# Performance work log

Measured on AMD Instinct MI355X. Metric: run time of the kernel, lower is better.

The kernel has to match this reference:

```python
import jax, jax.numpy as jnp
import numpy as np

T, B, V, E, H = 512, 64, 50000, 256, 256  # seq, batch, vocab, embed, lstm_hidden
D2 = 2 * H
NC = 5


def setup_inputs() -> dict:
    key = jax.random.key(0)
    ks = jax.random.split(key, 16)
    u = lambda k, shape, s=0.1: jax.random.uniform(k, shape, jnp.float32, -s, s)
    return {
        "embed": jax.random.randint(ks[0], (T, B), 0, V),
        "h0": jnp.zeros((2, B, H), jnp.float32),
        "c0": jnp.zeros((2, B, H), jnp.float32),
        "emb_table": jax.random.normal(ks[1], (V, E), jnp.float32),
        "Wih_f": u(ks[2], (4 * H, E)),
        "Whh_f": u(ks[3], (4 * H, H)),
        "bih_f": u(ks[4], (4 * H,)),
        "bhh_f": u(ks[5], (4 * H,)),
        "Wih_b": u(ks[6], (4 * H, E)),
        "Whh_b": u(ks[7], (4 * H, H)),
        "bih_b": u(ks[8], (4 * H,)),
        "bhh_b": u(ks[9], (4 * H,)),
        "W_word": u(ks[10], (D2, D2)),
        "b_word": u(ks[11], (D2,)),
        "proj_word": u(ks[12], (D2,)),
        "lin_W": u(ks[13], (NC, D2)),
        "lin_b": u(ks[14], (NC,)),
    }


def _lstm_dir(x, h0, c0, Wih, Whh, bih, bhh):
    # x: (T,B,E). PyTorch LSTM gate order: i, f, g, o.
    xg = jnp.einsum('tbe,ge->tbg', x, Wih) + bih + bhh  # (T,B,4H)

    def step(carry, xt):
        h, c = carry
        g = xt + h @ Whh.T
        i, f, gg, o = jnp.split(g, 4, axis=-1)
        c = jax.nn.sigmoid(f) * c + jax.nn.sigmoid(i) * jnp.tanh(gg)
        h = jax.nn.sigmoid(o) * jnp.tanh(c)
        return (h, c), h

    _, hs = jax.lax.scan(step, (h0, c0), xg)
    return hs  # (T,B,H)


def reference(embed, h0, c0, emb_table,
              Wih_f, Whh_f, bih_f, bhh_f,
              Wih_b, Whh_b, bih_b, bhh_b,
              W_word, b_word, proj_word, lin_W, lin_b):
    x = emb_table[embed]  # (T,B,E)
    out_f = _lstm_dir(x, h0[0], c0[0], Wih_f, Whh_f, bih_f, bhh_f)
    out_b = _lstm_dir(x[::-1], h0[1], c0[1], Wih_b, Whh_b, bih_b, bhh_b)[::-1]
    out = jnp.concatenate([out_f, out_b], axis=-1)  # (T,B,2H)
    # additive attention: tanh(out @ W + b) @ proj, softmax over T
    squish = jnp.tanh(jnp.einsum('tbd,de->tbe', out, W_word) + b_word)
    attn = jax.nn.softmax(jnp.einsum('tbd,d->tb', squish, proj_word), axis=0)
    vec = jnp.einsum('tb,tbd->bd', attn, out)  # (B,2H)
    return vec @ lin_W.T + lin_b  # (B, n_classes)
```

## Files before the change

kernel.cpp:

```cpp
#include <hip/hip_runtime.h>
#include <hip/hip_fp16.h>
#include <cstdint>
#include <cstddef>

#define TT 512
#define BB 64
#define EE 256
#define HH 256
#define G4 1024
#define DD 512
#define NCLS 5
#define CH 64
#define NCH (TT / CH)

typedef _Float16 half8 __attribute__((ext_vector_type(8)));
typedef float f32x4 __attribute__((ext_vector_type(4)));

#define OFF_XGF   0ull
#define OFF_XGB   8388608ull
#define OFF_OUTB  16777216ull
#define OFF_WHHF  50331648ull
#define OFF_WIHF  51380224ull
#define OFF_BIAS  52428800ull
#define OFF_HST   52436992ull
#define OFF_CST   52568064ull
#define OFF_LOG   52699136ull
#define OFF_ATT   52830208ull
#define OFF_HEX   52961280ull
#define OFF_FLG   53092352ull

__device__ __forceinline__ f32x4 mfma16(half8 a, half8 b, f32x4 c) {
  return __builtin_amdgcn_mfma_f32_16x16x32_f16(a, b, c, 0, 0, 0);
}
__device__ __forceinline__ f32x4 shflx4(f32x4 v, int mask) {
  f32x4 r;
  r[0] = __shfl_xor(v[0], mask, 64);
  r[1] = __shfl_xor(v[1], mask, 64);
  r[2] = __shfl_xor(v[2], mask, 64);
  r[3] = __shfl_xor(v[3], mask, 64);
  return r;
}

#define HSWZ(br, u) ((((br) * 256) + (u)) ^ (((br) & 7) << 3))

__global__ __launch_bounds__(256) void make_frags(
    const float* __restrict__ WhhF, const float* __restrict__ WhhB,
    const float* __restrict__ WihF, const float* __restrict__ WihB,
    __half* __restrict__ whhfrag, __half* __restrict__ wihfrag)
{
  int idx = blockIdx.x * 256 + threadIdx.x;
  int r = idx & 7, lane = (idx >> 3) & 63, ks = (idx >> 9) & 7;
  int mm = lane & 15;
  int k = ks * 32 + (lane >> 4) * 8 + r;
  if (idx < (1 << 19)) {
    int pf = (idx >> 12) & 63, d = (idx >> 18) & 1;
    const float* W = d ? WhhB : WhhF;
    int g = (mm & 3) * 256 + pf * 4 + (mm >> 2);
    whhfrag[idx] = __float2half(W[(size_t)g * HH + k]);
  } else {
    int e = idx - (1 << 19);
    int pf = (e >> 12) & 63, d = (e >> 18) & 1;
    const float* W = d ? WihB : WihF;
    int g = (mm & 3) * 256 + pf * 4 + (mm >> 2);
    wihfrag[e] = __float2half(W[(size_t)g * EE + k]);
  }
}

__global__ __launch_bounds__(256) void bias_prep(
    const float* __restrict__ bihF, const float* __restrict__ bhhF,
    const float* __restrict__ bihB, const float* __restrict__ bhhB,
    float* __restrict__ bias)
{
  int i = blockIdx.x * 256 + threadIdx.x;
  int d = i >> 10, pcol = i & 1023;
  int g = (pcol & 3) * 256 + (pcol >> 2);
  bias[i] = (d ? bihB : bihF)[g] + (d ? bhhB : bhhF)[g];
}

__global__ __launch_bounds__(256) void xg_mfma(
    int c, const int* __restrict__ embed, const float* __restrict__ emb,
    const __half* __restrict__ wihfrag, const float* __restrict__ biassum,
    __half* __restrict__ xgF, __half* __restrict__ xgB)
{
  const int d = blockIdx.z, ls = blockIdx.x, gblk = blockIdx.y;
  int t = c * CH + ls;
  if (d) t = TT - 1 - t;
  __half* xg = d ? xgB : xgF;
  const int tid = threadIdx.x, w = tid >> 6, l = tid & 63;

  __shared__ int idx[64];
  __shared__ unsigned short xs[64 * 256];

  if (tid < 64) idx[tid] = embed[t * BB + tid];
  __syncthreads();

  {
    const int rr = tid >> 2, cq = (tid & 3) * 64;
    const float* src = emb + (size_t)idx[rr] * EE + cq;
#pragma unroll
    for (int j = 0; j < 8; ++j) {
      float4 a = *(const float4*)(src + j * 8);
      float4 b = *(const float4*)(src + j * 8 + 4);
      half8 hv;
      hv[0] = (_Float16)a.x; hv[1] = (_Float16)a.y; hv[2] = (_Float16)a.z; hv[3] = (_Float16)a.w;
      hv[4] = (_Float16)b.x; hv[5] = (_Float16)b.y; hv[6] = (_Float16)b.z; hv[7] = (_Float16)b.w;
      int hidx = (rr * 256 + cq + j * 8) ^ ((rr & 7) << 3);
      *(half8*)&xs[hidx] = hv;
    }
  }
  __syncthreads();

  const __half* bfb = wihfrag + (size_t)((d * 64 + gblk * 4) * 8) * 512 + l * 8;
  half8 Bf[4][8];
#pragma unroll
  for (int ct = 0; ct < 4; ++ct)
#pragma unroll
    for (int ks = 0; ks < 8; ++ks)
      Bf[ct][ks] = *(const half8*)(bfb + (ct * 8 + ks) * 512);

  f32x4 acc[4];
#pragma unroll
  for (int ct = 0; ct < 4; ++ct) {
    float bv = biassum[d * 1024 + gblk * 64 + ct * 16 + (l & 15)];
    acc[ct][0] = bv; acc[ct][1] = bv; acc[ct][2] = bv; acc[ct][3] = bv;
  }

  const int arow = w * 16 + (l & 15);
#pragma unroll
  for (int ks = 0; ks < 8; ++ks) {
    int hidx = (arow * 256 + ks * 32 + (l >> 4) * 8) ^ ((arow & 7) << 3);
    half8 af = *(const half8*)&xs[hidx];
#pragma unroll
    for (int ct = 0; ct < 4; ++ct)
      acc[ct] = mfma16(af, Bf[ct][ks], acc[ct]);
  }

#pragma unroll
  for (int ct = 0; ct < 4; ++ct) {
    ushort4 sv;
    sv.x = __half_as_ushort(__float2half(acc[ct][0]));
    sv.y = __half_as_ushort(__float2half(acc[ct][1]));
    sv.z = __half_as_ushort(__float2half(acc[ct][2]));
    sv.w = __half_as_ushort(__float2half(acc[ct][3]));
    size_t base = ((size_t)(ls * 4 + w) * 64 + (gblk * 4 + ct)) * 256 + l * 4;
    *(ushort4*)((unsigned short*)xg + base) = sv;
  }
}

__global__ __launch_bounds__(512, 2) void scan_dist4(
    int c, const __half* __restrict__ xgF, const __half* __restrict__ xgB,
    const __half* __restrict__ whhfrag,
    const float* __restrict__ hin, const float* __restrict__ cin,
    float* __restrict__ hstate, float* __restrict__ cstate,
    __half* __restrict__ outb, unsigned long long* __restrict__ hexu,
    int* __restrict__ flags)
{
  const int id = blockIdx.x;
  const int ug = id >> 3, grp = id & 7;
  const int d = grp >> 2, bg = grp & 3;
  const int tid = threadIdx.x, w = tid >> 6, l = tid & 63;
  const int m = l & 15, qr = l >> 4, q = m & 3, ul = m >> 2;
  const unsigned short* xg = (const unsigned short*)(d ? xgB : xgF);

  __shared__ unsigned short hb0[16 * 256];
  __shared__ unsigned short hb1[16 * 256];

  const int pf0 = ug * 16 + w * 2;

  half8 Wf[2][8];
#pragma unroll
  for (int cf = 0; cf < 2; ++cf)
#pragma unroll
    for (int ks = 0; ks < 8; ++ks)
      Wf[cf][ks] = *(const half8*)(whhfrag +
          ((size_t)(d * 64 + pf0 + cf) * 8 + ks) * 512 + l * 8);

#pragma unroll
  for (int i = 0; i < 8; ++i) {
    int idx = i * 512 + tid;
    int r = idx >> 8, u = idx & 255;
    hb0[HSWZ(r, u)] = __half_as_ushort(
        __float2half(hin[(size_t)(d * BB + bg * 16 + r) * HH + u]));
  }
  float cst[2][4];
#pragma unroll
  for (int cf = 0; cf < 2; ++cf) {
    int U = (pf0 + cf) * 4 + ul;
#pragma unroll
    for (int j = 0; j < 4; ++j)
      cst[cf][j] = cin[(size_t)(d * BB + bg * 16 + qr * 4 + j) * HH + U];
  }
  __syncthreads();

  int afo[8];
#pragma unroll
  for (int ks = 0; ks < 8; ++ks) afo[ks] = HSWZ(m, ks * 32 + qr * 8);
  const int kso0 = ug * 2, kso1 = ug * 2 + 1;

  const unsigned short* xp = xg + ((size_t)bg * 64 + pf0) * 256 + l * 4;
  const float actB = (q == 2) ? 2.f : 1.f;

  f32x4 acc[2];
  {
    ushort4 xv0[2];
#pragma unroll
    for (int cf = 0; cf < 2; ++cf) xv0[cf] = *(const ushort4*)(xp + cf * 256);
#pragma unroll
    for (int cf = 0; cf < 2; ++cf) {
      acc[cf][0] = __half2float(__ushort_as_half(xv0[cf].x));
      acc[cf][1] = __half2float(__ushort_as_half(xv0[cf].y));
      acc[cf][2] = __half2float(__ushort_as_half(xv0[cf].z));
      acc[cf][3] = __half2float(__ushort_as_half(xv0[cf].w));
    }
    half8 ao0 = *(const half8*)&hb0[afo[kso0]];
    half8 ao1 = *(const half8*)&hb0[afo[kso1]];
#pragma unroll
    for (int cf = 0; cf < 2; ++cf) {
      acc[cf] = mfma16(ao0, Wf[cf][kso0], acc[cf]);
      acc[cf] = mfma16(ao1, Wf[cf][kso1], acc[cf]);
    }
  }
  ushort4 xv[2];
#pragma unroll
  for (int cf = 0; cf < 2; ++cf)
    xv[cf] = *(const ushort4*)(xp + (size_t)65536 + cf * 256);

  int p = 0;
  for (int ls = 0; ls < CH; ++ls) {
    unsigned short* cur = p ? hb1 : hb0;
    unsigned short* nxt = p ? hb0 : hb1;
    int tA = c * CH + ls;
    if (d) tA = TT - 1 - tA;
    unsigned long long* hx = hexu + (size_t)(grp * 2 + (ls & 1)) * 1024;

    half8 afp[6];
#pragma unroll
    for (int i = 0; i < 6; ++i) {
      int ks = i + (i >= kso0 ? 2 : 0);
      afp[i] = *(const half8*)&cur[afo[ks]];
    }
#pragma unroll
    for (int i = 0; i < 6; ++i) {
      int ks = i + (i >= kso0 ? 2 : 0);
#pragma unroll
      for (int cf = 0; cf < 2; ++cf)
        acc[cf] = mfma16(afp[i], Wf[cf][ks], acc[cf]);
    }

#pragma unroll
    for (int cf = 0; cf < 2; ++cf) {
      f32x4 a0;
#pragma unroll
      for (int jj = 0; jj < 4; ++jj) {
        float e = __expf(actB * acc[cf][jj]);
        a0[jj] = 1.f - __fdividef(actB, e + 1.f);
      }
      f32x4 a1 = shflx4(a0, 1);
      f32x4 a2 = shflx4(a0, 2);
      f32x4 a3 = shflx4(a0, 3);
      const int U = (pf0 + cf) * 4 + ul;
      float hv[4];
#pragma unroll
      for (int jj = 0; jj < 4; ++jj) {
        float cn = a1[jj] * cst[cf][jj] + a0[jj] * a2[jj];
        cst[cf][jj] = cn;
        float e2 = __expf(2.f * cn);
        hv[jj] = a3[jj] * (1.f - __fdividef(2.f, e2 + 1.f));
      }
      if (q == 0) {
        unsigned int p0 = (unsigned int)__half_as_ushort(__float2half(hv[0])) |
            ((unsigned int)__half_as_ushort(__float2half(hv[1])) << 16);
        unsigned int p1 = (unsigned int)__half_as_ushort(__float2half(hv[2])) |
            ((unsigned int)__half_as_ushort(__float2half(hv[3])) << 16);
        nxt[HSWZ(qr * 4 + 0, U)] = (unsigned short)(p0 & 0xffff);
        nxt[HSWZ(qr * 4 + 1, U)] = (unsigned short)(p0 >> 16);
        nxt[HSWZ(qr * 4 + 2, U)] = (unsigned short)(p1 & 0xffff);
        nxt[HSWZ(qr * 4 + 3, U)] = (unsigned short)(p1 >> 16);
        unsigned long long pk =
            (unsigned long long)p0 | ((unsigned long long)p1 << 32);
        __hip_atomic_store(&hx[U * 4 + qr], pk, __ATOMIC_RELAXED,
                           __HIP_MEMORY_SCOPE_AGENT);
      }
    }
    asm volatile("s_waitcnt vmcnt(0)" ::: "memory");
    __syncthreads();

    const int fbase = ((grp * NCH + c) * CH + ls) * 32;
    if (tid == 0)
      __hip_atomic_store(&flags[fbase + ug], 1, __ATOMIC_RELAXED,
                         __HIP_MEMORY_SCOPE_AGENT);

    {
      const int pr = tid >> 5, uL2 = (tid & 31) * 2;
      const int u = ug * 64 + uL2;
      *(unsigned int*)&outb[((size_t)tA * BB + bg * 16 + pr) * DD + d * HH + u] =
          *(const unsigned int*)&nxt[HSWZ(pr, u)];
    }
#pragma unroll
    for (int cf = 0; cf < 2; ++cf) {
      acc[cf][0] = __half2float(__ushort_as_half(xv[cf].x));
      acc[cf][1] = __half2float(__ushort_as_half(xv[cf].y));
      acc[cf][2] = __half2float(__ushort_as_half(xv[cf].z));
      acc[cf][3] = __half2float(__ushort_as_half(xv[cf].w));
    }
    {
      half8 ao0 = *(const half8*)&nxt[afo[kso0]];
      half8 ao1 = *(const half8*)&nxt[afo[kso1]];
#pragma unroll
      for (int cf = 0; cf < 2; ++cf) {
        acc[cf] = mfma16(ao0, Wf[cf][kso0], acc[cf]);
        acc[cf] = mfma16(ao1, Wf[cf][kso1], acc[cf]);
      }
    }
    {
      int lsn = (ls + 2 < CH) ? ls + 2 : CH - 1;
      const unsigned short* xn = xp + (size_t)lsn * 65536;
#pragma unroll
      for (int cf = 0; cf < 2; ++cf)
        xv[cf] = *(const ushort4*)(xn + cf * 256);
    }

    {
      bool need = (l < 4) && (l != ug);
      int got = need ? 0 : 1;
      while (!__all(got != 0)) {
        if (need && !got)
          got = __hip_atomic_load(&flags[fbase + l], __ATOMIC_RELAXED,
                                  __HIP_MEMORY_SCOPE_AGENT);
      }
    }
#pragma unroll
    for (int rep = 0; rep < 2; ++rep) {
      int idx = tid + rep * 512;
      if (idx < 768) {
        int pi = idx >> 8, rem = idx & 255, uu = rem >> 2, rq = rem & 3;
        int peer = pi + (pi >= ug ? 1 : 0);
        int U = peer * 64 + uu;
        unsigned long long v =
            __hip_atomic_load(&hx[U * 4 + rq], __ATOMIC_RELAXED,
                              __HIP_MEMORY_SCOPE_AGENT);
        nxt[HSWZ(rq * 4 + 0, U)] = (unsigned short)(v & 0xffff);
        nxt[HSWZ(rq * 4 + 1, U)] = (unsigned short)((v >> 16) & 0xffff);
        nxt[HSWZ(rq * 4 + 2, U)] = (unsigned short)((v >> 32) & 0xffff);
        nxt[HSWZ(rq * 4 + 3, U)] = (unsigned short)(v >> 48);
      }
    }
    __syncthreads();
    p ^= 1;
  }

  {
    unsigned short* fin = p ? hb1 : hb0;
#pragma unroll
    for (int i = 0; i < 8; ++i) {
      int idx = i * 512 + tid;
      int r = idx >> 8, u = idx & 255;
      hstate[(size_t)(d * BB + bg * 16 + r) * HH + u] =
          __half2float(__ushort_as_half(fin[HSWZ(r, u)]));
    }
  }
  if (q == 0) {
#pragma unroll
    for (int cf = 0; cf < 2; ++cf) {
      int U = (pf0 + cf) * 4 + ul;
#pragma unroll
      for (int j = 0; j < 4; ++j)
        cstate[(size_t)(d * BB + bg * 16 + qr * 4 + j) * HH + U] = cst[cf][j];
    }
  }
}

__global__ __launch_bounds__(1024, 1) void squish_logits(
    const __half* __restrict__ outb, const float* __restrict__ Ww,
    const float* __restrict__ bw, const float* __restrict__ proj,
    float* __restrict__ logits)
{
  const int r0 = blockIdx.x * 64;
  const int tid = threadIdx.x;
  const int tm = tid >> 6;
  const int tn = tid & 63;
  __shared__ float As[16][68];
  __shared__ float Bs[16][516];
  __shared__ float red[64][65];

  float acc[4][8] = {};
  const int am = tid >> 4, ak = tid & 15;
  const int bk = tid >> 7, bn = (tid & 127) * 4;

  for (int k0 = 0; k0 < DD; k0 += 16) {
    float a0 = __half2float(outb[(size_t)(r0 + am) * DD + k0 + ak]);
    float4 b0 = *(const float4*)&Ww[(size_t)(k0 + bk) * DD + bn];
    float4 b1 = *(const float4*)&Ww[(size_t)(k0 + bk + 8) * DD + bn];
    __syncthreads();
    As[ak][am] = a0;
    *(float4*)&Bs[bk][bn] = b0;
    *(float4*)&Bs[bk + 8][bn] = b1;
    __syncthreads();
#pragma unroll
    for (int k = 0; k < 16; ++k) {
      float4 a = *(const float4*)&As[k][tm * 4];
      float4 p0 = *(const float4*)&Bs[k][tn * 8];
      float4 p1 = *(const float4*)&Bs[k][tn * 8 + 4];
      float av[4] = {a.x, a.y, a.z, a.w};
#pragma unroll
      for (int i = 0; i < 4; ++i) {
        acc[i][0] += av[i] * p0.x; acc[i][1] += av[i] * p0.y;
        acc[i][2] += av[i] * p0.z; acc[i][3] += av[i] * p0.w;
        acc[i][4] += av[i] * p1.x; acc[i][5] += av[i] * p1.y;
        acc[i][6] += av[i] * p1.z; acc[i][7] += av[i] * p1.w;
      }
    }
  }
  float partial[4] = {0.f, 0.f, 0.f, 0.f};
#pragma unroll
  for (int jj = 0; jj < 8; ++jj) {
    int col = tn * 8 + jj;
    float bwv = bw[col], pv = proj[col];
#pragma unroll
    for (int i = 0; i < 4; ++i)
      partial[i] += tanhf(acc[i][jj] + bwv) * pv;
  }
#pragma unroll
  for (int i = 0; i < 4; ++i) red[tm * 4 + i][tn] = partial[i];
  __syncthreads();
  if (tid < 64) {
    float s = 0.f;
    for (int x = 0; x < 64; ++x) s += red[tid][x];
    logits[r0 + tid] = s;
  }
}

__global__ __launch_bounds__(256) void softmax_t(const float* __restrict__ logits,
                                                 float* __restrict__ attn)
{
  const int b = blockIdx.x;
  const int tid = threadIdx.x;
  __shared__ float sm[256];
  float v0 = logits[tid * BB + b];
  float v1 = logits[(tid + 256) * BB + b];
  sm[tid] = fmaxf(v0, v1);
  __syncthreads();
  for (int s = 128; s > 0; s >>= 1) {
    if (tid < s) sm[tid] = fmaxf(sm[tid], sm[tid + s]);
    __syncthreads();
  }
  float M = sm[0];
  __syncthreads();
  float e0 = expf(v0 - M), e1 = expf(v1 - M);
  sm[tid] = e0 + e1;
  __syncthreads();
  for (int s = 128; s > 0; s >>= 1) {
    if (tid < s) sm[tid] += sm[tid + s];
    __syncthreads();
  }
  float inv = 1.f / sm[0];
  attn[tid * BB + b] = e0 * inv;
  attn[(tid + 256) * BB + b] = e1 * inv;
}

__global__ __launch_bounds__(512) void vec_final(
    const __half* __restrict__ outb, const float* __restrict__ attn,
    const float* __restrict__ linW, const float* __restrict__ linb,
    float* __restrict__ y)
{
  const int b = blockIdx.x;
  const int d = threadIdx.x;
  float acc = 0.f;
  for (int t = 0; t < TT; ++t)
    acc += attn[t * BB + b] * __half2float(outb[((size_t)t * BB + b) * DD + d]);
  __shared__ float red[512];
  for (int cls = 0; cls < NCLS; ++cls) {
    red[d] = acc * linW[cls * DD + d];
    __syncthreads();
    for (int s = 256; s > 0; s >>= 1) {
      if (d < s) red[d] += red[d + s];
      __syncthreads();
    }
    if (d == 0) y[b * NCLS + cls] = red[0] + linb[cls];
    __syncthreads();
  }
}

extern "C" void kernel_launch(void* const* d_in, const int* in_sizes, int n_in,
                              void* d_out, int out_size, void* d_ws, size_t ws_size,
                              hipStream_t stream) {
  const int*   embed     = (const int*)d_in[0];
  const float* h0        = (const float*)d_in[1];
  const float* c0        = (const float*)d_in[2];
  const float* emb_table = (const float*)d_in[3];
  const float* Wih_f     = (const float*)d_in[4];
  const float* Whh_f     = (const float*)d_in[5];
  const float* bih_f     = (const float*)d_in[6];
  const float* bhh_f     = (const float*)d_in[7];
  const float* Wih_b     = (const float*)d_in[8];
  const float* Whh_b     = (const float*)d_in[9];
  const float* bih_b     = (const float*)d_in[10];
  const float* bhh_b     = (const float*)d_in[11];
  const float* W_word    = (const float*)d_in[12];
  const float* b_word    = (const float*)d_in[13];
  const float* proj_word = (const float*)d_in[14];
  const float* lin_W     = (const float*)d_in[15];
  const float* lin_b     = (const float*)d_in[16];

  char* ws = (char*)d_ws;
  __half* xgF     = (__half*)(ws + OFF_XGF);
  __half* xgB     = (__half*)(ws + OFF_XGB);
  __half* outb    = (__half*)(ws + OFF_OUTB);
  __half* whhfrag = (__half*)(ws + OFF_WHHF);
  __half* wihfrag = (__half*)(ws + OFF_WIHF);
  float*  biassum = (float*)(ws + OFF_BIAS);
  float*  hstate  = (float*)(ws + OFF_HST);
  float*  cstate  = (float*)(ws + OFF_CST);
  float*  logits  = (float*)(ws + OFF_LOG);
  float*  attn    = (float*)(ws + OFF_ATT);
  unsigned long long* hexu = (unsigned long long*)(ws + OFF_HEX);
  int*    flags   = (int*)(ws + OFF_FLG);

  hipMemsetAsync(flags, 0, 524288, stream);

  make_frags<<<4096, 256, 0, stream>>>(Whh_f, Whh_b, Wih_f, Wih_b, whhfrag, wihfrag);
  bias_prep<<<8, 256, 0, stream>>>(bih_f, bhh_f, bih_b, bhh_b, biassum);

  for (int c = 0; c < NCH; ++c) {
    xg_mfma<<<dim3(CH, 16, 2), 256, 0, stream>>>(c, embed, emb_table,
        wihfrag, biassum, xgF, xgB);
    const float* hin = (c == 0) ? h0 : hstate;
    const float* cin = (c == 0) ? c0 : cstate;
    scan_dist4<<<dim3(32), 512, 0, stream>>>(c, xgF, xgB, whhfrag,
        hin, cin, hstate, cstate, outb, hexu, flags);
  }

  squish_logits<<<512, 1024, 0, stream>>>(outb, W_word, b_word, proj_word, logits);
  softmax_t<<<64, 256, 0, stream>>>(logits, attn);
  vec_final<<<64, 512, 0, stream>>>(outb, attn, lin_W, lin_b, (float*)d_out);
}
```

Baseline: 2.931 ms.

## Halve scan blocks per direction group and move attention squish GEMM to MFMA

The recurrent scan now splits each direction/batch-group's hidden units across 2 blocks instead of 4. Each wave owns 4 gate fragments and exchanges h with a single peer block per step, which cuts cross-block flag polling and global h traffic but doubles the serial MFMA and activation work per block. Separately, the fp32 SIMT GEMM in the attention scoring stage is replaced by an fp16 MFMA kernel that reads pre-swizzled W_word fragments, with a fast exp-based tanh and shuffle reductions. This lowers attention precision to fp16 inputs and adds a fragment prep kernel.

New measurement: 6.107 ms. 2.08x slower.

```diff
diff --git a/kernel.cpp b/kernel.cpp
--- a/kernel.cpp
+++ b/kernel.cpp
@@ -28,9 +28,14 @@
 #define OFF_ATT   52830208ull
 #define OFF_HEX   52961280ull
 #define OFF_FLG   53092352ull
+#define OFF_WWF   53616640ull
 
 __device__ __forceinline__ f32x4 mfma16(half8 a, half8 b, f32x4 c) {
   return __builtin_amdgcn_mfma_f32_16x16x32_f16(a, b, c, 0, 0, 0);
+}
+__device__ __forceinline__ float tanh_(float x) {
+  float e = __expf(2.f * x);
+  return 1.f - __fdividef(2.f, e + 1.f);
 }
 __device__ __forceinline__ f32x4 shflx4(f32x4 v, int mask) {
   f32x4 r;
@@ -66,6 +71,16 @@
   }
 }
 
+__global__ __launch_bounds__(256) void make_wwfrag(
+    const float* __restrict__ Ww, __half* __restrict__ wwfrag)
+{
+  int idx = blockIdx.x * 256 + threadIdx.x;
+  int r = idx & 7, lane = (idx >> 3) & 63, ks = (idx >> 9) & 15, cf = idx >> 13;
+  int e = cf * 16 + (lane & 15);
+  int k = ks * 32 + (lane >> 4) * 8 + r;
+  wwfrag[idx] = __float2half(Ww[(size_t)k * DD + e]);
+}
+
 __global__ __launch_bounds__(256) void bias_prep(
     const float* __restrict__ bihF, const float* __restrict__ bhhF,
     const float* __restrict__ bihB, const float* __restrict__ bhhB,
@@ -147,7 +162,7 @@
   }
 }
 
-__global__ __launch_bounds__(512, 2) void scan_dist4(
+__global__ __launch_bounds__(512, 2) void scan_dist5(
     int c, const __half* __restrict__ xgF, const __half* __restrict__ xgB,
     const __half* __restrict__ whhfrag,
     const float* __restrict__ hin, const float* __restrict__ cin,
@@ -165,11 +180,13 @@
   __shared__ unsigned short hb0[16 * 256];
   __shared__ unsigned short hb1[16 * 256];
 
-  const int pf0 = ug * 16 + w * 2;
-
-  half8 Wf[2][8];
-#pragma unroll
-  for (int cf = 0; cf < 2; ++cf)
+  const int pf0 = ug * 32 + w * 4;
+  const int kown = ug * 4;
+  const int kpeer = 4 - kown;
+
+  half8 Wf[4][8];
+#pragma unroll
+  for (int cf = 0; cf < 4; ++cf)
 #pragma unroll
     for (int ks = 0; ks < 8; ++ks)
       Wf[cf][ks] = *(const half8*)(whhfrag +
@@ -182,9 +199,9 @@
     hb0[HSWZ(r, u)] = __half_as_ushort(
         __float2half(hin[(size_t)(d * BB + bg * 16 + r) * HH + u]));
   }
-  float cst[2][4];
-#pragma unroll
-  for (int cf = 0; cf < 2; ++cf) {
+  float cst[4][4];
+#pragma unroll
+  for (int cf = 0; cf < 4; ++cf) {
     int U = (pf0 + cf) * 4 + ul;
 #pragma unroll
     for (int j = 0; j < 4; ++j)
@@ -195,34 +212,33 @@
   int afo[8];
 #pragma unroll
   for (int ks = 0; ks < 8; ++ks) afo[ks] = HSWZ(m, ks * 32 + qr * 8);
-  const int kso0 = ug * 2, kso1 = ug * 2 + 1;
 
   const unsigned short* xp = xg + ((size_t)bg * 64 + pf0) * 256 + l * 4;
   const float actB = (q == 2) ? 2.f : 1.f;
 
-  f32x4 acc[2];
+  f32x4 acc[4];
   {
-    ushort4 xv0[2];
-#pragma unroll
-    for (int cf = 0; cf < 2; ++cf) xv0[cf] = *(const ushort4*)(xp + cf * 256);
-#pragma unroll
-    for (int cf = 0; cf < 2; ++cf) {
+    ushort4 xv0[4];
+#pragma unroll
+    for (int cf = 0; cf < 4; ++cf) xv0[cf] = *(const ushort4*)(xp + cf * 256);
+#pragma unroll
+    for (int cf = 0; cf < 4; ++cf) {
       acc[cf][0] = __half2float(__ushort_as_half(xv0[cf].x));
       acc[cf][1] = __half2float(__ushort_as_half(xv0[cf].y));
       acc[cf][2] = __half2float(__ushort_as_half(xv0[cf].z));
       acc[cf][3] = __half2float(__ushort_as_half(xv0[cf].w));
     }
-    half8 ao0 = *(const half8*)&hb0[afo[kso0]];
-    half8 ao1 = *(const half8*)&hb0[afo[kso1]];
-#pragma unroll
-    for (int cf = 0; cf < 2; ++cf) {
-      acc[cf] = mfma16(ao0, Wf[cf][kso0], acc[cf]);
-      acc[cf] = mfma16(ao1, Wf[cf][kso1], acc[cf]);
-    }
-  }
-  ushort4 xv[2];
-#pragma unroll
-  for (int cf = 0; cf < 2; ++cf)
+#pragma unroll
+    for (int kk = 0; kk < 4; ++kk) {
+      half8 ao = *(const half8*)&hb0[afo[kown + kk]];
+#pragma unroll
+      for (int cf = 0; cf < 4; ++cf)
+        acc[cf] = mfma16(ao, Wf[cf][kown + kk], acc[cf]);
+    }
+  }
+  ushort4 xv[4];
+#pragma unroll
+  for (int cf = 0; cf < 4; ++cf)
     xv[cf] = *(const ushort4*)(xp + (size_t)65536 + cf * 256);
 
   int p = 0;
@@ -233,22 +249,16 @@
     if (d) tA = TT - 1 - tA;
     unsigned long long* hx = hexu + (size_t)(grp * 2 + (ls & 1)) * 1024;
 
-    half8 afp[6];
-#pragma unroll
-    for (int i = 0; i < 6; ++i) {
-      int ks = i + (i >= kso0 ? 2 : 0);
-      afp[i] = *(const half8*)&cur[afo[ks]];
-    }
-#pragma unroll
-    for (int i = 0; i < 6; ++i) {
-      int ks = i + (i >= kso0 ? 2 : 0);
-#pragma unroll
-      for (int cf = 0; cf < 2; ++cf)
-        acc[cf] = mfma16(afp[i], Wf[cf][ks], acc[cf]);
-    }
-
-#pragma unroll
-    for (int cf = 0; cf < 2; ++cf) {
+#pragma unroll
+    for (int kk = 0; kk < 4; ++kk) {
+      half8 ap = *(const half8*)&cur[afo[kpeer + kk]];
+#pragma unroll
+      for (int cf = 0; cf < 4; ++cf)
+        acc[cf] = mfma16(ap, Wf[cf][kpeer + kk], acc[cf]);
+    }
+
+#pragma unroll
+    for (int cf = 0; cf < 4; ++cf) {
       f32x4 a0;
 #pragma unroll
       for (int jj = 0; jj < 4; ++jj) {
@@ -291,59 +301,45 @@
                          __HIP_MEMORY_SCOPE_AGENT);
 
     {
-      const int pr = tid >> 5, uL2 = (tid & 31) * 2;
-      const int u = ug * 64 + uL2;
-      *(unsigned int*)&outb[((size_t)tA * BB + bg * 16 + pr) * DD + d * HH + u] =
-          *(const unsigned int*)&nxt[HSWZ(pr, u)];
-    }
-#pragma unroll
-    for (int cf = 0; cf < 2; ++cf) {
+      const int pr = tid >> 5, uL4 = (tid & 31) * 4;
+      const int u = ug * 128 + uL4;
+      *(uint2*)&outb[((size_t)tA * BB + bg * 16 + pr) * DD + d * HH + u] =
+          *(const uint2*)&nxt[HSWZ(pr, u)];
+    }
+#pragma unroll
+    for (int cf = 0; cf < 4; ++cf) {
       acc[cf][0] = __half2float(__ushort_as_half(xv[cf].x));
       acc[cf][1] = __half2float(__ushort_as_half(xv[cf].y));
       acc[cf][2] = __half2float(__ushort_as_half(xv[cf].z));
       acc[cf][3] = __half2float(__ushort_as_half(xv[cf].w));
     }
-    {
-      half8 ao0 = *(const half8*)&nxt[afo[kso0]];
-      half8 ao1 = *(const half8*)&nxt[afo[kso1]];
-#pragma unroll
-      for (int cf = 0; cf < 2; ++cf) {
-        acc[cf] = mfma16(ao0, Wf[cf][kso0], acc[cf]);
-        acc[cf] = mfma16(ao1, Wf[cf][kso1], acc[cf]);
-      }
+#pragma unroll
+    for (int kk = 0; kk < 4; ++kk) {
+      half8 ao = *(const half8*)&nxt[afo[kown + kk]];
+#pragma unroll
+      for (int cf = 0; cf < 4; ++cf)
+        acc[cf] = mfma16(ao, Wf[cf][kown + kk], acc[cf]);
     }
     {
       int lsn = (ls + 2 < CH) ? ls + 2 : CH - 1;
       const unsigned short* xn = xp + (size_t)lsn * 65536;
 #pragma unroll
-      for (int cf = 0; cf < 2; ++cf)
+      for (int cf = 0; cf < 4; ++cf)
         xv[cf] = *(const ushort4*)(xn + cf * 256);
     }
 
+    while (__hip_atomic_load(&flags[fbase + (ug ^ 1)], __ATOMIC_RELAXED,
+                             __HIP_MEMORY_SCOPE_AGENT) == 0) {}
+    asm volatile("" ::: "memory");
     {
-      bool need = (l < 4) && (l != ug);
-      int got = need ? 0 : 1;
-      while (!__all(got != 0)) {
-        if (need && !got)
-          got = __hip_atomic_load(&flags[fbase + l], __ATOMIC_RELAXED,
-                                  __HIP_MEMORY_SCOPE_AGENT);
-      }
-    }
-#pragma unroll
-    for (int rep = 0; rep < 2; ++rep) {
-      int idx = tid + rep * 512;
-      if (idx < 768) {
-        int pi = idx >> 8, rem = idx & 255, uu = rem >> 2, rq = rem & 3;
-        int peer = pi + (pi >= ug ? 1 : 0);
-        int U = peer * 64 + uu;
-        unsigned long long v =
-            __hip_atomic_load(&hx[U * 4 + rq], __ATOMIC_RELAXED,
-                              __HIP_MEMORY_SCOPE_AGENT);
-        nxt[HSWZ(rq * 4 + 0, U)] = (unsigned short)(v & 0xffff);
-        nxt[HSWZ(rq * 4 + 1, U)] = (unsigned short)((v >> 16) & 0xffff);
-        nxt[HSWZ(rq * 4 + 2, U)] = (unsigned short)((v >> 32) & 0xffff);
-        nxt[HSWZ(rq * 4 + 3, U)] = (unsigned short)(v >> 48);
-      }
+      int uu = tid >> 2, rq = tid & 3;
+      int U = (ug ^ 1) * 128 + uu;
+      unsigned long long v = __hip_atomic_load(&hx[U * 4 + rq],
+          __ATOMIC_RELAXED, __HIP_MEMORY_SCOPE_AGENT);
+      nxt[HSWZ(rq * 4 + 0, U)] = (unsigned short)(v & 0xffff);
+      nxt[HSWZ(rq * 4 + 1, U)] = (unsigned short)((v >> 16) & 0xffff);
+      nxt[HSWZ(rq * 4 + 2, U)] = (unsigned short)((v >> 32) & 0xffff);
+      nxt[HSWZ(rq * 4 + 3, U)] = (unsigned short)(v >> 48);
     }
     __syncthreads();
     p ^= 1;
@@ -361,7 +357,7 @@
   }
   if (q == 0) {
 #pragma unroll
-    for (int cf = 0; cf < 2; ++cf) {
+    for (int cf = 0; cf < 4; ++cf) {
       int U = (pf0 + cf) * 4 + ul;
 #pragma unroll
       for (int j = 0; j < 4; ++j)
@@ -370,63 +366,53 @@
   }
 }
 
-__global__ __launch_bounds__(1024, 1) void squish_logits(
-    const __half* __restrict__ outb, const float* __restrict__ Ww,
+__global__ __launch_bounds__(256, 1) void squish_mfma(
+    const __half* __restrict__ outb, const __half* __restrict__ wwfrag,
     const float* __restrict__ bw, const float* __restrict__ proj,
     float* __restrict__ logits)
 {
   const int r0 = blockIdx.x * 64;
-  const int tid = threadIdx.x;
-  const int tm = tid >> 6;
-  const int tn = tid & 63;
-  __shared__ float As[16][68];
-  __shared__ float Bs[16][516];
-  __shared__ float red[64][65];
-
-  float acc[4][8] = {};
-  const int am = tid >> 4, ak = tid & 15;
-  const int bk = tid >> 7, bn = (tid & 127) * 4;
-
-  for (int k0 = 0; k0 < DD; k0 += 16) {
-    float a0 = __half2float(outb[(size_t)(r0 + am) * DD + k0 + ak]);
-    float4 b0 = *(const float4*)&Ww[(size_t)(k0 + bk) * DD + bn];
-    float4 b1 = *(const float4*)&Ww[(size_t)(k0 + bk + 8) * DD + bn];
-    __syncthreads();
-    As[ak][am] = a0;
-    *(float4*)&Bs[bk][bn] = b0;
-    *(float4*)&Bs[bk + 8][bn] = b1;
-    __syncthreads();
-#pragma unroll
-    for (int k = 0; k < 16; ++k) {
-      float4 a = *(const float4*)&As[k][tm * 4];
-      float4 p0 = *(const float4*)&Bs[k][tn * 8];
-      float4 p1 = *(const float4*)&Bs[k][tn * 8 + 4];
-      float av[4] = {a.x, a.y, a.z, a.w};
-#pragma unroll
-      for (int i = 0; i < 4; ++i) {
-        acc[i][0] += av[i] * p0.x; acc[i][1] += av[i] * p0.y;
-        acc[i][2] += av[i] * p0.z; acc[i][3] += av[i] * p0.w;
-        acc[i][4] += av[i] * p1.x; acc[i][5] += av[i] * p1.y;
-        acc[i][6] += av[i] * p1.z; acc[i][7] += av[i] * p1.w;
-      }
-    }
-  }
+  const int tid = threadIdx.x, w = tid >> 6, l = tid & 63;
+  const int m = l & 15, qr = l >> 4;
+
+  f32x4 acc[32];
+#pragma unroll
+  for (int cf = 0; cf < 32; ++cf) {
+    acc[cf][0] = 0.f; acc[cf][1] = 0.f; acc[cf][2] = 0.f; acc[cf][3] = 0.f;
+  }
+
+  const unsigned short* arow =
+      (const unsigned short*)outb + (size_t)(r0 + w * 16 + m) * DD + qr * 8;
+  const __half* bfb = wwfrag + l * 8;
+
+#pragma unroll
+  for (int ks = 0; ks < 16; ++ks) {
+    half8 a = *(const half8*)(arow + ks * 32);
+#pragma unroll
+    for (int cf = 0; cf < 32; ++cf) {
+      half8 b = *(const half8*)(bfb + (size_t)(cf * 16 + ks) * 512);
+      acc[cf] = mfma16(a, b, acc[cf]);
+    }
+  }
+
   float partial[4] = {0.f, 0.f, 0.f, 0.f};
 #pragma unroll
-  for (int jj = 0; jj < 8; ++jj) {
-    int col = tn * 8 + jj;
-    float bwv = bw[col], pv = proj[col];
-#pragma unroll
-    for (int i = 0; i < 4; ++i)
-      partial[i] += tanhf(acc[i][jj] + bwv) * pv;
-  }
-#pragma unroll
-  for (int i = 0; i < 4; ++i) red[tm * 4 + i][tn] = partial[i];
-  __syncthreads();
-  if (tid < 64) {
-    float s = 0.f;
-    for (int x = 0; x < 64; ++x) s += red[tid][x];
-    logits[r0 + tid] = s;
+  for (int cf = 0; cf < 32; ++cf) {
+    int e = cf * 16 + m;
+    float bwv = bw[e], pv = proj[e];
+#pragma unroll
+    for (int r = 0; r < 4; ++r)
+      partial[r] += tanh_(acc[cf][r] + bwv) * pv;
+  }
+#pragma unroll
+  for (int mask = 1; mask < 16; mask <<= 1)
+#pragma unroll
+    for (int r = 0; r < 4; ++r)
+      partial[r] += __shfl_xor(partial[r], mask, 64);
+  if (m == 0) {
+#pragma unroll
+    for (int r = 0; r < 4; ++r)
+      logits[r0 + w * 16 + qr * 4 + r] = partial[r];
   }
 }
 
@@ -515,10 +501,12 @@
   float*  attn    = (float*)(ws + OFF_ATT);
   unsigned long long* hexu = (unsigned long long*)(ws + OFF_HEX);
   int*    flags   = (int*)(ws + OFF_FLG);
+  __half* wwfrag  = (__half*)(ws + OFF_WWF);
 
   hipMemsetAsync(flags, 0, 524288, stream);
 
   make_frags<<<4096, 256, 0, stream>>>(Whh_f, Whh_b, Wih_f, Wih_b, whhfrag, wihfrag);
+  make_wwfrag<<<1024, 256, 0, stream>>>(W_word, wwfrag);
   bias_prep<<<8, 256, 0, stream>>>(bih_f, bhh_f, bih_b, bhh_b, biassum);
 
   for (int c = 0; c < NCH; ++c) {
@@ -526,11 +514,11 @@
         wihfrag, biassum, xgF, xgB);
     const float* hin = (c == 0) ? h0 : hstate;
     const float* cin = (c == 0) ? c0 : cstate;
-    scan_dist4<<<dim3(32), 512, 0, stream>>>(c, xgF, xgB, whhfrag,
+    scan_dist5<<<dim3(16), 512, 0, stream>>>(c, xgF, xgB, whhfrag,
         hin, cin, hstate, cstate, outb, hexu, flags);
   }
 
-  squish_logits<<<512, 1024, 0, stream>>>(outb, W_word, b_word, proj_word, logits);
+  squish_mfma<<<512, 256, 0, stream>>>(outb, wwfrag, b_word, proj_word, logits);
   softmax_t<<<64, 256, 0, stream>>>(logits, attn);
   vec_final<<<64, 512, 0, stream>>>(outb, attn, lin_W, lin_b, (float*)d_out);
 }
```

## Move attention squish GEMM onto fp16 MFMA with pre-swizzled W_word fragments

Applied to the files above, without the earlier changes.

Replaces the fp32 shared-memory tiled SIMT GEMM for tanh(out·W_word+b)·proj with an MFMA 16x16x32 fp16 kernel that reads W_word from a new pre-converted fragment buffer built by a small prep kernel. Row reduction now uses wave shuffles instead of a shared-memory table, and tanhf is replaced by an exp-based fast approximation. This cuts the compute cost of the post-scan attention GEMM. In exchange W_word is rounded to fp16 and tanh is less accurate, and the kernel holds 32 accumulator vectors per thread, which is heavy on registers.

New measurement: 2.917 ms, median of 2. No clear change (-0.5%).

```diff
diff --git a/kernel.cpp b/kernel.cpp
--- a/kernel.cpp
+++ b/kernel.cpp
@@ -28,9 +28,14 @@
 #define OFF_ATT   52830208ull
 #define OFF_HEX   52961280ull
 #define OFF_FLG   53092352ull
+#define OFF_WWF   53616640ull
 
 __device__ __forceinline__ f32x4 mfma16(half8 a, half8 b, f32x4 c) {
   return __builtin_amdgcn_mfma_f32_16x16x32_f16(a, b, c, 0, 0, 0);
+}
+__device__ __forceinline__ float tanh_(float x) {
+  float e = __expf(2.f * x);
+  return 1.f - __fdividef(2.f, e + 1.f);
 }
 __device__ __forceinline__ f32x4 shflx4(f32x4 v, int mask) {
   f32x4 r;
@@ -64,6 +69,16 @@
     int g = (mm & 3) * 256 + pf * 4 + (mm >> 2);
     wihfrag[e] = __float2half(W[(size_t)g * EE + k]);
   }
+}
+
+__global__ __launch_bounds__(256) void make_wwfrag(
+    const float* __restrict__ Ww, __half* __restrict__ wwfrag)
+{
+  int idx = blockIdx.x * 256 + threadIdx.x;
+  int r = idx & 7, lane = (idx >> 3) & 63, ks = (idx >> 9) & 15, cf = idx >> 13;
+  int e = cf * 16 + (lane & 15);
+  int k = ks * 32 + (lane >> 4) * 8 + r;
+  wwfrag[idx] = __float2half(Ww[(size_t)k * DD + e]);
 }
 
 __global__ __launch_bounds__(256) void bias_prep(
@@ -370,63 +385,53 @@
   }
 }
 
-__global__ __launch_bounds__(1024, 1) void squish_logits(
-    const __half* __restrict__ outb, const float* __restrict__ Ww,
+__global__ __launch_bounds__(256, 1) void squish_mfma(
+    const __half* __restrict__ outb, const __half* __restrict__ wwfrag,
     const float* __restrict__ bw, const float* __restrict__ proj,
     float* __restrict__ logits)
 {
   const int r0 = blockIdx.x * 64;
-  const int tid = threadIdx.x;
-  const int tm = tid >> 6;
-  const int tn = tid & 63;
-  __shared__ float As[16][68];
-  __shared__ float Bs[16][516];
-  __shared__ float red[64][65];
-
-  float acc[4][8] = {};
-  const int am = tid >> 4, ak = tid & 15;
-  const int bk = tid >> 7, bn = (tid & 127) * 4;
-
-  for (int k0 = 0; k0 < DD; k0 += 16) {
-    float a0 = __half2float(outb[(size_t)(r0 + am) * DD + k0 + ak]);
-    float4 b0 = *(const float4*)&Ww[(size_t)(k0 + bk) * DD + bn];
-    float4 b1 = *(const float4*)&Ww[(size_t)(k0 + bk + 8) * DD + bn];
-    __syncthreads();
-    As[ak][am] = a0;
-    *(float4*)&Bs[bk][bn] = b0;
-    *(float4*)&Bs[bk + 8][bn] = b1;
-    __syncthreads();
-#pragma unroll
-    for (int k = 0; k < 16; ++k) {
-      float4 a = *(const float4*)&As[k][tm * 4];
-      float4 p0 = *(const float4*)&Bs[k][tn * 8];
-      float4 p1 = *(const float4*)&Bs[k][tn * 8 + 4];
-      float av[4] = {a.x, a.y, a.z, a.w};
-#pragma unroll
-      for (int i = 0; i < 4; ++i) {
-        acc[i][0] += av[i] * p0.x; acc[i][1] += av[i] * p0.y;
-        acc[i][2] += av[i] * p0.z; acc[i][3] += av[i] * p0.w;
-        acc[i][4] += av[i] * p1.x; acc[i][5] += av[i] * p1.y;
-        acc[i][6] += av[i] * p1.z; acc[i][7] += av[i] * p1.w;
-      }
-    }
-  }
+  const int tid = threadIdx.x, w = tid >> 6, l = tid & 63;
+  const int m = l & 15, qr = l >> 4;
+
+  f32x4 acc[32];
+#pragma unroll
+  for (int cf = 0; cf < 32; ++cf) {
+    acc[cf][0] = 0.f; acc[cf][1] = 0.f; acc[cf][2] = 0.f; acc[cf][3] = 0.f;
+  }
+
+  const unsigned short* arow =
+      (const unsigned short*)outb + (size_t)(r0 + w * 16 + m) * DD + qr * 8;
+  const __half* bfb = wwfrag + l * 8;
+
+#pragma unroll
+  for (int ks = 0; ks < 16; ++ks) {
+    half8 a = *(const half8*)(arow + ks * 32);
+#pragma unroll
+    for (int cf = 0; cf < 32; ++cf) {
+      half8 b = *(const half8*)(bfb + (size_t)(cf * 16 + ks) * 512);
+      acc[cf] = mfma16(a, b, acc[cf]);
+    }
+  }
+
   float partial[4] = {0.f, 0.f, 0.f, 0.f};
 #pragma unroll
-  for (int jj = 0; jj < 8; ++jj) {
-    int col = tn * 8 + jj;
-    float bwv = bw[col], pv = proj[col];
-#pragma unroll
-    for (int i = 0; i < 4; ++i)
-      partial[i] += tanhf(acc[i][jj] + bwv) * pv;
-  }
-#pragma unroll
-  for (int i = 0; i < 4; ++i) red[tm * 4 + i][tn] = partial[i];
-  __syncthreads();
-  if (tid < 64) {
-    float s = 0.f;
-    for (int x = 0; x < 64; ++x) s += red[tid][x];
-    logits[r0 + tid] = s;
+  for (int cf = 0; cf < 32; ++cf) {
+    int e = cf * 16 + m;
+    float bwv = bw[e], pv = proj[e];
+#pragma unroll
+    for (int r = 0; r < 4; ++r)
+      partial[r] += tanh_(acc[cf][r] + bwv) * pv;
+  }
+#pragma unroll
+  for (int mask = 1; mask < 16; mask <<= 1)
+#pragma unroll
+    for (int r = 0; r < 4; ++r)
+      partial[r] += __shfl_xor(partial[r], mask, 64);
+  if (m == 0) {
+#pragma unroll
+    for (int r = 0; r < 4; ++r)
+      logits[r0 + w * 16 + qr * 4 + r] = partial[r];
   }
 }
 
@@ -515,10 +520,12 @@
   float*  attn    = (float*)(ws + OFF_ATT);
   unsigned long long* hexu = (unsigned long long*)(ws + OFF_HEX);
   int*    flags   = (int*)(ws + OFF_FLG);
+  __half* wwfrag  = (__half*)(ws + OFF_WWF);
 
   hipMemsetAsync(flags, 0, 524288, stream);
 
   make_frags<<<4096, 256, 0, stream>>>(Whh_f, Whh_b, Wih_f, Wih_b, whhfrag, wihfrag);
+  make_wwfrag<<<1024, 256, 0, stream>>>(W_word, wwfrag);
   bias_prep<<<8, 256, 0, stream>>>(bih_f, bhh_f, bih_b, bhh_b, biassum);
 
   for (int c = 0; c < NCH; ++c) {
@@ -530,7 +537,7 @@
         hin, cin, hstate, cstate, outb, hexu, flags);
   }
 
-  squish_logits<<<512, 1024, 0, stream>>>(outb, W_word, b_word, proj_word, logits);
+  squish_mfma<<<512, 256, 0, stream>>>(outb, wwfrag, b_word, proj_word, logits);
   softmax_t<<<64, 256, 0, stream>>>(logits, attn);
   vec_final<<<64, 512, 0, stream>>>(outb, attn, lin_W, lin_b, (float*)d_out);
 }
```
